# Kernel optimization log

Hardware: AMD Instinct MI355X
Metric: run time of the kernel (lower is better)

## Reference

```python
import jax, jax.numpy as jnp
import numpy as np
from jax import lax

N, L, E, ED, H = 100000, 48, 1600000, 17, 48

def _lin_init(k, fan_in, fan_out):
    kw, kb = jax.random.split(k)
    s = 1.0 / np.sqrt(fan_in)
    W = jax.random.uniform(kw, (fan_in, fan_out), minval=-s, maxval=s, dtype=jnp.float32)
    b = jax.random.uniform(kb, (fan_out,), minval=-s, maxval=s, dtype=jnp.float32)
    return W, b

def setup_inputs() -> dict:
    key = jax.random.key(0)
    ks = jax.random.split(key, 10)
    nodes = jax.random.normal(ks[0], (N, L, 1), dtype=jnp.float32)
    edge_index = jax.random.randint(ks[1], (2, E), 0, N, dtype=jnp.int64) if jax.config.jax_enable_x64 else jax.random.randint(ks[1], (2, E), 0, N, dtype=jnp.int32)
    edge_attr = jax.random.normal(ks[2], (E, ED), dtype=jnp.float32)
    valid = (jax.random.uniform(ks[3], (1, N, L)) < 0.8).astype(jnp.float32)
    r = jnp.zeros((1,), jnp.float32)
    fx = jnp.zeros((1,), jnp.float32)
    W1, b1 = _lin_init(ks[4], ED, H)   # lin_edge[0]
    W2, b2 = _lin_init(ks[5], H, H)    # lin_edge[2]
    Wg, bg = _lin_init(ks[6], H, H)    # gru[0]
    Ww, bw = _lin_init(ks[7], H, 1)    # weight_mlp
    Wf, bf = _lin_init(ks[8], 3, 1)    # fuse_mlp
    return {"nodes": nodes, "edge_index": edge_index, "edge_attr": edge_attr,
            "valid": valid, "r": r, "fx": fx,
            "W1": W1, "b1": b1, "W2": W2, "b2": b2, "Wg": Wg, "bg": bg,
            "Ww": Ww, "bw": bw, "Wf": Wf, "bf": bf}

def _gelu(x):
    return jax.nn.gelu(x, approximate=False)  # torch GELU default is exact erf

def reference(nodes, edge_index, edge_attr, valid, r, fx,
              W1, b1, W2, b2, Wg, bg, Ww, bw, Wf, bf):
    n = nodes.shape[0]
    # torch.no_grad block: mask nodes by valid, flatten (C==1)
    v = lax.stop_gradient(valid[0][..., None])            # [N, L, 1]
    x = lax.stop_gradient((nodes * v).reshape(n, L))      # [N, L]
    original = x
    nv_mask = (1.0 - v).reshape(n, L)                     # not_valid mask [N, L]
    src, dst = edge_index[0], edge_index[1]
    for _ in range(3):
        # lin_edge: 17 -> 48 -> GELU -> 48 -> ReLU  (per edge)
        eh = jax.nn.relu(_gelu(edge_attr @ W1 + b1) @ W2 + b2)      # [E, 48]
        xc = jnp.concatenate([x, v[..., 0]], axis=-1)               # [N, 2L]
        x_j = xc[src]                                               # gather [E, 2L]
        g = _gelu(eh @ Wg + bg)                                     # gru
        w = g @ Ww + bw                                             # [E, 1]
        w = jnp.mean(x_j[:, L:], axis=-1, keepdims=True) * w
        msg = x_j * jax.nn.sigmoid(w)                               # [E, 2L]
        agg = jax.ops.segment_sum(msg, dst, num_segments=n)         # scatter-add [N, 2L]
        new_half = agg[:, :L]                                       # [N, L]
        nn3 = jnp.stack([new_half, x, nv_mask], axis=-1)            # [N, L, 3]
        mask = jax.nn.sigmoid((nn3 @ Wf + bf)[..., 0])              # [N, L]
        x = (1.0 - mask) * x + nv_mask * mask * new_half
        v = jnp.logical_or((original != x)[..., None], v > 0).astype(jnp.float32)
        v = v.at[:, 0].set(0.0)
        nv_mask = (1.0 - v).reshape(n, L)
    return x[0][None]  # [1, L]
```

## Files before the change

kernel.cpp:

```cpp
#include <hip/hip_runtime.h>
#include <math.h>

#define NN 100000
#define LF 48
#define NE 1600000
#define EDIMS 17
#define MASKW 3125
#define CAP_E 16384
#define MAXLOC 12288

static_assert(NN == MASKW * 32, "mask width");
static_assert((CAP_E & (CAP_E - 1)) == 0, "CAP_E pow2");

__device__ __forceinline__ float gelu_f(float x) {
    return 0.5f * x * (1.0f + erff(x * 0.7071067811865475f));
}
__device__ __forceinline__ float sigm_f(float x) {
    return 1.0f / (1.0f + expf(-x));
}

__global__ void seed_kernel(unsigned* __restrict__ M3) {
    if (threadIdx.x == 0 && blockIdx.x == 0) M3[0] = 1u;
}

__global__ void expand_kernel(const int* __restrict__ src, const int* __restrict__ dst,
                              const unsigned* __restrict__ Min, unsigned* __restrict__ Mout,
                              int4* __restrict__ list, int* __restrict__ counter)
{
    int e = blockIdx.x * 256 + threadIdx.x;
    if (e >= NE) return;
    int d = dst[e];
    if (Min[d >> 5] & (1u << (d & 31))) {
        int s = src[e];
        int idx = atomicAdd(counter, 1);
        if (idx < CAP_E) list[idx] = make_int4(s, d, e, 0);
        atomicOr(&Mout[s >> 5], 1u << (s & 31));
    }
}

__global__ void compact_kernel(const unsigned* __restrict__ M0, int* __restrict__ n2l,
                               int* __restrict__ l2n, int* __restrict__ nloc)
{
    int w = blockIdx.x * 256 + threadIdx.x;
    if (w >= MASKW) return;
    unsigned bits = M0[w];
    while (bits) {
        int b = __ffs(bits) - 1;
        bits &= bits - 1;
        int node = w * 32 + b;
        int loc = atomicAdd(nloc, 1);
        if (loc < MAXLOC) { n2l[node] = loc; l2n[loc] = node; }
    }
}

__global__ void init_kernel(const int* __restrict__ nloc_p, const int* __restrict__ l2n,
                            const float* __restrict__ nodes, const float* __restrict__ valid,
                            float* __restrict__ X0, float* __restrict__ V0, float* __restrict__ MV0)
{
    int loc = blockIdx.x * 256 + threadIdx.x;
    int nl = *nloc_p; if (nl > MAXLOC) nl = MAXLOC;
    if (loc >= nl) return;
    int node = l2n[loc];
    float sum = 0.f;
    #pragma unroll 4
    for (int l = 0; l < LF; ++l) {
        float v = valid[node * LF + l];
        float x = nodes[node * LF + l] * v;
        X0[loc * LF + l] = x;
        V0[loc * LF + l] = v;
        sum += v;
    }
    MV0[loc] = sum * (1.0f / 48.0f);
}

__global__ void w0_kernel(int4* __restrict__ lists, const int* __restrict__ counts,
                          const int* __restrict__ n2l, const float* __restrict__ ea_g,
                          const float* __restrict__ W1, const float* __restrict__ b1,
                          const float* __restrict__ W2, const float* __restrict__ b2,
                          const float* __restrict__ Wg, const float* __restrict__ bg,
                          const float* __restrict__ Ww, const float* __restrict__ bw)
{
    int t = blockIdx.x >> 14;
    int i = blockIdx.x & (CAP_E - 1);
    int c = counts[t]; if (c > CAP_E) c = CAP_E;
    if (i >= c) return;
    int4 ent = lists[t * CAP_E + i];
    __shared__ float sh[64];
    __shared__ float eas[EDIMS];
    int lane = threadIdx.x;
    if (lane < EDIMS) eas[lane] = ea_g[(long)ent.z * EDIMS + lane];
    __syncthreads();
    float h1 = 0.f;
    if (lane < 48) {
        float acc = b1[lane];
        #pragma unroll
        for (int k = 0; k < EDIMS; ++k) acc += eas[k] * W1[k * 48 + lane];
        h1 = gelu_f(acc);
    }
    sh[lane] = h1;
    __syncthreads();
    float h2 = 0.f;
    if (lane < 48) {
        float acc = b2[lane];
        #pragma unroll 8
        for (int k = 0; k < 48; ++k) acc += sh[k] * W2[k * 48 + lane];
        h2 = fmaxf(acc, 0.f);
    }
    __syncthreads();
    sh[lane] = h2;
    __syncthreads();
    float part = 0.f;
    if (lane < 48) {
        float acc = bg[lane];
        #pragma unroll 8
        for (int k = 0; k < 48; ++k) acc += sh[k] * Wg[k * 48 + lane];
        part = gelu_f(acc) * Ww[lane];
    }
    #pragma unroll
    for (int offd = 32; offd > 0; offd >>= 1) part += __shfl_down(part, offd, 64);
    if (lane == 0) {
        float w0 = part + bw[0];
        int sl = n2l[ent.x]; if ((unsigned)sl >= MAXLOC) sl = 0;
        int dl = n2l[ent.y]; if ((unsigned)dl >= MAXLOC) dl = 0;
        lists[t * CAP_E + i] = make_int4(sl, dl, ent.z, __float_as_int(w0));
    }
}

__global__ void edge_agg_kernel(const int4* __restrict__ list, const int* __restrict__ count_p,
                                const float* __restrict__ Xprev, const float* __restrict__ MVprev,
                                float* __restrict__ agg)
{
    int gid = blockIdx.x * 256 + threadIdx.x;
    int i = gid >> 6, lane = gid & 63;
    int c = *count_p; if (c > CAP_E) c = CAP_E;
    if (i >= c || lane >= 48) return;
    int4 ent = list[i];
    if ((unsigned)ent.x >= MAXLOC || (unsigned)ent.y >= MAXLOC) return;
    float s = sigm_f(MVprev[ent.x] * __int_as_float(ent.w));
    atomicAdd(&agg[ent.y * 48 + lane], s * Xprev[ent.x * 48 + lane]);
}

__global__ void node_update_kernel(const int* __restrict__ nloc_p, const int* __restrict__ l2n,
                                   const unsigned* __restrict__ Mt,
                                   const float* __restrict__ agg, const float* __restrict__ Xprev,
                                   const float* __restrict__ Vprev, const float* __restrict__ Xorig,
                                   float* __restrict__ Xcur, float* __restrict__ Vcur,
                                   float* __restrict__ MVcur,
                                   const float* __restrict__ Wf, const float* __restrict__ bf)
{
    int loc = blockIdx.x * 256 + threadIdx.x;
    int nl = *nloc_p; if (nl > MAXLOC) nl = MAXLOC;
    if (loc >= nl) return;
    int node = l2n[loc];
    if (!(Mt[node >> 5] & (1u << (node & 31)))) return;
    float wf0 = Wf[0], wf1 = Wf[1], wf2 = Wf[2], bfs = bf[0];
    float vsum = 0.f;
    #pragma unroll 4
    for (int l = 0; l < LF; ++l) {
        float nh = agg[loc * LF + l];
        float xo = Xprev[loc * LF + l];
        float vp = Vprev[loc * LF + l];
        float nv = 1.0f - vp;
        float m = sigm_f(nh * wf0 + xo * wf1 + nv * wf2 + bfs);
        float xn = (1.0f - m) * xo + nv * m * nh;
        float vn = ((Xorig[loc * LF + l] != xn) || (vp > 0.f)) ? 1.0f : 0.0f;
        if (l == 0) vn = 0.0f;
        Xcur[loc * LF + l] = xn;
        Vcur[loc * LF + l] = vn;
        vsum += vn;
    }
    MVcur[loc] = vsum * (1.0f / 48.0f);
}

__global__ void output_kernel(const int* __restrict__ n2l, const float* __restrict__ Xf,
                              float* __restrict__ out)
{
    int l = threadIdx.x;
    if (l < 48) out[l] = Xf[n2l[0] * 48 + l];
}

extern "C" void kernel_launch(void* const* d_in, const int* in_sizes, int n_in,
                              void* d_out, int out_size, void* d_ws, size_t ws_size,
                              hipStream_t stream)
{
    const float* nodes = (const float*)d_in[0];
    const int*   eidx  = (const int*)d_in[1];
    const float* eattr = (const float*)d_in[2];
    const float* valid = (const float*)d_in[3];
    const float* W1 = (const float*)d_in[6];
    const float* b1 = (const float*)d_in[7];
    const float* W2 = (const float*)d_in[8];
    const float* b2 = (const float*)d_in[9];
    const float* Wg = (const float*)d_in[10];
    const float* bg = (const float*)d_in[11];
    const float* Ww = (const float*)d_in[12];
    const float* bw = (const float*)d_in[13];
    const float* Wf = (const float*)d_in[14];
    const float* bf = (const float*)d_in[15];
    const int* src = eidx;
    const int* dst = eidx + NE;

    char* ws = (char*)d_ws;
    size_t off = 0;
    auto alloc = [&](size_t bytes) -> char* {
        char* p = ws + off;
        off += (bytes + 255) & ~(size_t)255;
        return p;
    };
    int*      counters = (int*)alloc(64);
    unsigned* M3 = (unsigned*)alloc(MASKW * 4);
    unsigned* M2 = (unsigned*)alloc(MASKW * 4);
    unsigned* M1 = (unsigned*)alloc(MASKW * 4);
    unsigned* M0 = (unsigned*)alloc(MASKW * 4);
    int*      n2l = (int*)alloc((size_t)NN * 4);
    int*      l2n = (int*)alloc((size_t)MAXLOC * 4);
    int4*     lists = (int4*)alloc((size_t)3 * CAP_E * 16);
    float*    X0 = (float*)alloc((size_t)MAXLOC * LF * 4);
    float*    XA = (float*)alloc((size_t)MAXLOC * LF * 4);
    float*    XB = (float*)alloc((size_t)MAXLOC * LF * 4);
    float*    VA = (float*)alloc((size_t)MAXLOC * LF * 4);
    float*    VB = (float*)alloc((size_t)MAXLOC * LF * 4);
    float*    MVA = (float*)alloc((size_t)MAXLOC * 4);
    float*    MVB = (float*)alloc((size_t)MAXLOC * 4);
    float*    agg = (float*)alloc((size_t)MAXLOC * LF * 4);
    if (off > ws_size) return;

    hipMemsetAsync(counters, 0, 64, stream);
    hipMemsetAsync(M3, 0, MASKW * 4, stream);
    hipMemsetAsync(M2, 0, MASKW * 4, stream);
    hipMemsetAsync(M1, 0, MASKW * 4, stream);
    hipMemsetAsync(M0, 0, MASKW * 4, stream);
    seed_kernel<<<1, 64, 0, stream>>>(M3);

    hipMemcpyAsync(M2, M3, MASKW * 4, hipMemcpyDeviceToDevice, stream);
    expand_kernel<<<NE / 256, 256, 0, stream>>>(src, dst, M3, M2, lists + 0 * CAP_E, counters + 0);
    hipMemcpyAsync(M1, M2, MASKW * 4, hipMemcpyDeviceToDevice, stream);
    expand_kernel<<<NE / 256, 256, 0, stream>>>(src, dst, M2, M1, lists + 1 * CAP_E, counters + 1);
    hipMemcpyAsync(M0, M1, MASKW * 4, hipMemcpyDeviceToDevice, stream);
    expand_kernel<<<NE / 256, 256, 0, stream>>>(src, dst, M1, M0, lists + 2 * CAP_E, counters + 2);

    compact_kernel<<<(MASKW + 255) / 256, 256, 0, stream>>>(M0, n2l, l2n, counters + 3);
    init_kernel<<<MAXLOC / 256, 256, 0, stream>>>(counters + 3, l2n, nodes, valid, X0, VA, MVA);
    w0_kernel<<<3 * CAP_E, 64, 0, stream>>>(lists, counters, n2l, eattr,
                                            W1, b1, W2, b2, Wg, bg, Ww, bw);

    const size_t aggBytes = (size_t)MAXLOC * LF * 4;
    hipMemsetAsync(agg, 0, aggBytes, stream);
    edge_agg_kernel<<<CAP_E * 64 / 256, 256, 0, stream>>>(lists + 2 * CAP_E, counters + 2, X0, MVA, agg);
    node_update_kernel<<<MAXLOC / 256, 256, 0, stream>>>(counters + 3, l2n, M1, agg, X0, VA, X0,
                                                         XA, VB, MVB, Wf, bf);
    hipMemsetAsync(agg, 0, aggBytes, stream);
    edge_agg_kernel<<<CAP_E * 64 / 256, 256, 0, stream>>>(lists + 1 * CAP_E, counters + 1, XA, MVB, agg);
    node_update_kernel<<<MAXLOC / 256, 256, 0, stream>>>(counters + 3, l2n, M2, agg, XA, VB, X0,
                                                         XB, VA, MVA, Wf, bf);
    hipMemsetAsync(agg, 0, aggBytes, stream);
    edge_agg_kernel<<<CAP_E * 64 / 256, 256, 0, stream>>>(lists + 0 * CAP_E, counters + 0, XB, MVA, agg);
    node_update_kernel<<<MAXLOC / 256, 256, 0, stream>>>(counters + 3, l2n, M3, agg, XB, VA, X0,
                                                         XA, VB, MVB, Wf, bf);

    output_kernel<<<1, 64, 0, stream>>>(n2l, XA, (float*)d_out);
}
```

Baseline: 351.0 us.

## Fuse all phases into one cooperative persistent kernel with grid syncs

```diff
diff --git a/kernel.cpp b/kernel.cpp
--- a/kernel.cpp
+++ b/kernel.cpp
@@ -1,5 +1,8 @@
 #include <hip/hip_runtime.h>
+#include <hip/hip_cooperative_groups.h>
 #include <math.h>
+
+namespace cg = cooperative_groups;
 
 #define NN 100000
 #define LF 48
@@ -8,10 +11,25 @@
 #define MASKW 3125
 #define CAP_E 16384
 #define MAXLOC 12288
+#define BLK 256
+#define GRID_MAX 1024
 
 static_assert(NN == MASKW * 32, "mask width");
 static_assert((CAP_E & (CAP_E - 1)) == 0, "CAP_E pow2");
 
+struct Params {
+    const float* nodes; const float* valid; const float* eattr;
+    const int* src; const int* dst;
+    const float *W1, *b1, *W2, *b2, *Wg, *bg, *Ww, *bw, *Wf, *bf;
+    int* counters;
+    unsigned *M3, *M2, *M1, *M0;
+    int *n2l, *l2n;
+    int4* lists;
+    float *X0, *XA, *XB, *VA, *VB, *MVA, *MVB;
+    float *agg;
+    float* out;
+};
+
 __device__ __forceinline__ float gelu_f(float x) {
     return 0.5f * x * (1.0f + erff(x * 0.7071067811865475f));
 }
@@ -19,244 +37,252 @@
     return 1.0f / (1.0f + expf(-x));
 }
 
-__global__ void seed_kernel(unsigned* __restrict__ M3) {
-    if (threadIdx.x == 0 && blockIdx.x == 0) M3[0] = 1u;
-}
-
-__global__ void expand_kernel(const int* __restrict__ src, const int* __restrict__ dst,
-                              const unsigned* __restrict__ Min, unsigned* __restrict__ Mout,
-                              int4* __restrict__ list, int* __restrict__ counter)
-{
-    int e = blockIdx.x * 256 + threadIdx.x;
-    if (e >= NE) return;
-    int d = dst[e];
-    if (Min[d >> 5] & (1u << (d & 31))) {
-        int s = src[e];
-        int idx = atomicAdd(counter, 1);
-        if (idx < CAP_E) list[idx] = make_int4(s, d, e, 0);
-        atomicOr(&Mout[s >> 5], 1u << (s & 31));
-    }
-}
-
-__global__ void compact_kernel(const unsigned* __restrict__ M0, int* __restrict__ n2l,
-                               int* __restrict__ l2n, int* __restrict__ nloc)
-{
-    int w = blockIdx.x * 256 + threadIdx.x;
-    if (w >= MASKW) return;
-    unsigned bits = M0[w];
-    while (bits) {
-        int b = __ffs(bits) - 1;
-        bits &= bits - 1;
-        int node = w * 32 + b;
-        int loc = atomicAdd(nloc, 1);
-        if (loc < MAXLOC) { n2l[node] = loc; l2n[loc] = node; }
-    }
-}
-
-__global__ void init_kernel(const int* __restrict__ nloc_p, const int* __restrict__ l2n,
-                            const float* __restrict__ nodes, const float* __restrict__ valid,
-                            float* __restrict__ X0, float* __restrict__ V0, float* __restrict__ MV0)
-{
-    int loc = blockIdx.x * 256 + threadIdx.x;
-    int nl = *nloc_p; if (nl > MAXLOC) nl = MAXLOC;
-    if (loc >= nl) return;
-    int node = l2n[loc];
-    float sum = 0.f;
-    #pragma unroll 4
-    for (int l = 0; l < LF; ++l) {
-        float v = valid[node * LF + l];
-        float x = nodes[node * LF + l] * v;
-        X0[loc * LF + l] = x;
-        V0[loc * LF + l] = v;
-        sum += v;
-    }
-    MV0[loc] = sum * (1.0f / 48.0f);
-}
-
-__global__ void w0_kernel(int4* __restrict__ lists, const int* __restrict__ counts,
-                          const int* __restrict__ n2l, const float* __restrict__ ea_g,
-                          const float* __restrict__ W1, const float* __restrict__ b1,
-                          const float* __restrict__ W2, const float* __restrict__ b2,
-                          const float* __restrict__ Wg, const float* __restrict__ bg,
-                          const float* __restrict__ Ww, const float* __restrict__ bw)
-{
-    int t = blockIdx.x >> 14;
-    int i = blockIdx.x & (CAP_E - 1);
-    int c = counts[t]; if (c > CAP_E) c = CAP_E;
-    if (i >= c) return;
-    int4 ent = lists[t * CAP_E + i];
-    __shared__ float sh[64];
-    __shared__ float eas[EDIMS];
-    int lane = threadIdx.x;
-    if (lane < EDIMS) eas[lane] = ea_g[(long)ent.z * EDIMS + lane];
-    __syncthreads();
+
+__device__ void expand_phase(const Params& p, const unsigned* __restrict__ Min,
+                             unsigned* __restrict__ Mout, int4* __restrict__ list,
+                             int* __restrict__ counter, int tid, int nthr)
+{
+    for (int w = tid; w < MASKW; w += nthr) atomicOr(&Mout[w], Min[w]);
+    for (int e = tid; e < NE; e += nthr) {
+        int d = p.dst[e];
+        if (Min[d >> 5] & (1u << (d & 31))) {
+            int s = p.src[e];
+            int idx = atomicAdd(counter, 1);
+            if (idx < CAP_E) list[idx] = make_int4(s, d, e, 0);
+            atomicOr(&Mout[s >> 5], 1u << (s & 31));
+        }
+    }
+}
+
+__device__ void w0_edge(const Params& p, int4* __restrict__ entp, int lane)
+{
+    int4 ent = *entp;
+    float ea = 0.f;
+    if (lane < EDIMS) ea = p.eattr[(long)ent.z * EDIMS + lane];
     float h1 = 0.f;
     if (lane < 48) {
-        float acc = b1[lane];
+        float acc = p.b1[lane];
         #pragma unroll
-        for (int k = 0; k < EDIMS; ++k) acc += eas[k] * W1[k * 48 + lane];
+        for (int k = 0; k < EDIMS; ++k) acc += __shfl(ea, k, 64) * p.W1[k * 48 + lane];
         h1 = gelu_f(acc);
     }
-    sh[lane] = h1;
-    __syncthreads();
     float h2 = 0.f;
     if (lane < 48) {
-        float acc = b2[lane];
+        float acc = p.b2[lane];
         #pragma unroll 8
-        for (int k = 0; k < 48; ++k) acc += sh[k] * W2[k * 48 + lane];
+        for (int k = 0; k < 48; ++k) acc += __shfl(h1, k, 64) * p.W2[k * 48 + lane];
         h2 = fmaxf(acc, 0.f);
     }
-    __syncthreads();
-    sh[lane] = h2;
-    __syncthreads();
     float part = 0.f;
     if (lane < 48) {
-        float acc = bg[lane];
+        float acc = p.bg[lane];
         #pragma unroll 8
-        for (int k = 0; k < 48; ++k) acc += sh[k] * Wg[k * 48 + lane];
-        part = gelu_f(acc) * Ww[lane];
+        for (int k = 0; k < 48; ++k) acc += __shfl(h2, k, 64) * p.Wg[k * 48 + lane];
+        part = gelu_f(acc) * p.Ww[lane];
     }
     #pragma unroll
-    for (int offd = 32; offd > 0; offd >>= 1) part += __shfl_down(part, offd, 64);
+    for (int off = 32; off > 0; off >>= 1) part += __shfl_down(part, off, 64);
     if (lane == 0) {
-        float w0 = part + bw[0];
-        int sl = n2l[ent.x]; if ((unsigned)sl >= MAXLOC) sl = 0;
-        int dl = n2l[ent.y]; if ((unsigned)dl >= MAXLOC) dl = 0;
-        lists[t * CAP_E + i] = make_int4(sl, dl, ent.z, __float_as_int(w0));
-    }
-}
-
-__global__ void edge_agg_kernel(const int4* __restrict__ list, const int* __restrict__ count_p,
-                                const float* __restrict__ Xprev, const float* __restrict__ MVprev,
-                                float* __restrict__ agg)
-{
-    int gid = blockIdx.x * 256 + threadIdx.x;
-    int i = gid >> 6, lane = gid & 63;
-    int c = *count_p; if (c > CAP_E) c = CAP_E;
-    if (i >= c || lane >= 48) return;
-    int4 ent = list[i];
-    if ((unsigned)ent.x >= MAXLOC || (unsigned)ent.y >= MAXLOC) return;
-    float s = sigm_f(MVprev[ent.x] * __int_as_float(ent.w));
-    atomicAdd(&agg[ent.y * 48 + lane], s * Xprev[ent.x * 48 + lane]);
-}
-
-__global__ void node_update_kernel(const int* __restrict__ nloc_p, const int* __restrict__ l2n,
-                                   const unsigned* __restrict__ Mt,
-                                   const float* __restrict__ agg, const float* __restrict__ Xprev,
-                                   const float* __restrict__ Vprev, const float* __restrict__ Xorig,
-                                   float* __restrict__ Xcur, float* __restrict__ Vcur,
-                                   float* __restrict__ MVcur,
-                                   const float* __restrict__ Wf, const float* __restrict__ bf)
-{
-    int loc = blockIdx.x * 256 + threadIdx.x;
-    int nl = *nloc_p; if (nl > MAXLOC) nl = MAXLOC;
-    if (loc >= nl) return;
-    int node = l2n[loc];
-    if (!(Mt[node >> 5] & (1u << (node & 31)))) return;
-    float wf0 = Wf[0], wf1 = Wf[1], wf2 = Wf[2], bfs = bf[0];
-    float vsum = 0.f;
-    #pragma unroll 4
-    for (int l = 0; l < LF; ++l) {
-        float nh = agg[loc * LF + l];
-        float xo = Xprev[loc * LF + l];
-        float vp = Vprev[loc * LF + l];
-        float nv = 1.0f - vp;
-        float m = sigm_f(nh * wf0 + xo * wf1 + nv * wf2 + bfs);
-        float xn = (1.0f - m) * xo + nv * m * nh;
-        float vn = ((Xorig[loc * LF + l] != xn) || (vp > 0.f)) ? 1.0f : 0.0f;
-        if (l == 0) vn = 0.0f;
-        Xcur[loc * LF + l] = xn;
-        Vcur[loc * LF + l] = vn;
-        vsum += vn;
-    }
-    MVcur[loc] = vsum * (1.0f / 48.0f);
-}
-
-__global__ void output_kernel(const int* __restrict__ n2l, const float* __restrict__ Xf,
-                              float* __restrict__ out)
-{
-    int l = threadIdx.x;
-    if (l < 48) out[l] = Xf[n2l[0] * 48 + l];
+        float w0 = part + p.bw[0];
+        int sl = p.n2l[ent.x]; if ((unsigned)sl >= MAXLOC) sl = 0;
+        int dl = p.n2l[ent.y]; if ((unsigned)dl >= MAXLOC) dl = 0;
+        *entp = make_int4(sl, dl, ent.z, __float_as_int(w0));
+    }
+}
+
+__device__ void agg_phase(const Params& p, const int4* __restrict__ list,
+                          const int* __restrict__ cnt, const float* __restrict__ Xprev,
+                          const float* __restrict__ MVprev, float* __restrict__ agg,
+                          int tid, int nthr)
+{
+    int c = *cnt; if (c > CAP_E) c = CAP_E;
+    int lane = tid & 63;
+    for (int i = tid >> 6; i < c; i += (nthr >> 6)) {
+        int4 ent = list[i];
+        if ((unsigned)ent.x >= MAXLOC || (unsigned)ent.y >= MAXLOC) continue;
+        float s = sigm_f(MVprev[ent.x] * __int_as_float(ent.w));
+        if (lane < 48) atomicAdd(&agg[ent.y * LF + lane], s * Xprev[ent.x * LF + lane]);
+    }
+}
+
+__device__ void update_phase(const Params& p, const unsigned* __restrict__ Mt,
+                             const float* __restrict__ agg, const float* __restrict__ Xprev,
+                             const float* __restrict__ Vprev, float* __restrict__ Xcur,
+                             float* __restrict__ Vcur, float* __restrict__ MVcur,
+                             int tid, int nthr)
+{
+    int nl = p.counters[3]; if (nl > MAXLOC) nl = MAXLOC;
+    float wf0 = p.Wf[0], wf1 = p.Wf[1], wf2 = p.Wf[2], bfs = p.bf[0];
+    for (int loc = tid; loc < nl; loc += nthr) {
+        int node = p.l2n[loc];
+        if (!(Mt[node >> 5] & (1u << (node & 31)))) continue;
+        float vsum = 0.f;
+        #pragma unroll 4
+        for (int l = 0; l < LF; ++l) {
+            float nh = agg[loc * LF + l];
+            float xo = Xprev[loc * LF + l];
+            float vp = Vprev[loc * LF + l];
+            float nv = 1.0f - vp;
+            float m = sigm_f(nh * wf0 + xo * wf1 + nv * wf2 + bfs);
+            float xn = (1.0f - m) * xo + nv * m * nh;
+            float vn = ((p.X0[loc * LF + l] != xn) || (vp > 0.f)) ? 1.0f : 0.0f;
+            if (l == 0) vn = 0.0f;
+            Xcur[loc * LF + l] = xn;
+            Vcur[loc * LF + l] = vn;
+            vsum += vn;
+        }
+        MVcur[loc] = vsum * (1.0f / 48.0f);
+    }
+}
+
+__device__ void run_phase(const Params& p, int ph, int tid, int nthr)
+{
+    float* agg0 = p.agg;
+    float* agg1 = p.agg + MAXLOC * LF;
+    float* agg2 = p.agg + 2 * MAXLOC * LF;
+    switch (ph) {
+    case 0: {
+        if (tid < 4) p.counters[tid] = 0;
+        for (int i = tid; i < MASKW; i += nthr) {
+            p.M3[i] = (i == 0) ? 1u : 0u;
+            p.M2[i] = 0u; p.M1[i] = 0u; p.M0[i] = 0u;
+        }
+        for (int i = tid; i < 3 * MAXLOC * LF; i += nthr) p.agg[i] = 0.f;
+    } break;
+    case 1: expand_phase(p, p.M3, p.M2, p.lists + 0 * CAP_E, p.counters + 0, tid, nthr); break;
+    case 2: expand_phase(p, p.M2, p.M1, p.lists + 1 * CAP_E, p.counters + 1, tid, nthr); break;
+    case 3: expand_phase(p, p.M1, p.M0, p.lists + 2 * CAP_E, p.counters + 2, tid, nthr); break;
+    case 4: {
+        for (int w = tid; w < MASKW; w += nthr) {
+            unsigned bits = p.M0[w];
+            while (bits) {
+                int b = __ffs(bits) - 1;
+                bits &= bits - 1;
+                int node = w * 32 + b;
+                int loc = atomicAdd(p.counters + 3, 1);
+                if (loc < MAXLOC) { p.n2l[node] = loc; p.l2n[loc] = node; }
+            }
+        }
+    } break;
+    case 5: {
+        int nl = p.counters[3]; if (nl > MAXLOC) nl = MAXLOC;
+        for (int loc = tid; loc < nl; loc += nthr) {
+            int node = p.l2n[loc];
+            const float4* nv = (const float4*)(p.valid + (size_t)node * LF);
+            const float4* nx = (const float4*)(p.nodes + (size_t)node * LF);
+            float4* X0v = (float4*)(p.X0 + (size_t)loc * LF);
+            float4* V0v = (float4*)(p.VA + (size_t)loc * LF);
+            float sum = 0.f;
+            #pragma unroll
+            for (int k = 0; k < 12; ++k) {
+                float4 v = nv[k], x = nx[k];
+                x.x *= v.x; x.y *= v.y; x.z *= v.z; x.w *= v.w;
+                X0v[k] = x; V0v[k] = v;
+                sum += v.x + v.y + v.z + v.w;
+            }
+            p.MVA[loc] = sum * (1.0f / 48.0f);
+        }
+        int c0 = p.counters[0]; c0 = (c0 > CAP_E) ? CAP_E : c0;
+        int c1 = p.counters[1]; c1 = (c1 > CAP_E) ? CAP_E : c1;
+        int c2 = p.counters[2]; c2 = (c2 > CAP_E) ? CAP_E : c2;
+        int total = c0 + c1 + c2;
+        int lane = tid & 63;
+        for (int g = tid >> 6; g < total; g += (nthr >> 6)) {
+            int4* entp;
+            if (g < c0)           entp = p.lists + g;
+            else if (g < c0 + c1) entp = p.lists + CAP_E + (g - c0);
+            else                  entp = p.lists + 2 * CAP_E + (g - c0 - c1);
+            w0_edge(p, entp, lane);
+        }
+    } break;
+    case 6:  agg_phase(p, p.lists + 2 * CAP_E, p.counters + 2, p.X0, p.MVA, agg0, tid, nthr); break;
+    case 7:  update_phase(p, p.M1, agg0, p.X0, p.VA, p.XA, p.VB, p.MVB, tid, nthr); break;
+    case 8:  agg_phase(p, p.lists + 1 * CAP_E, p.counters + 1, p.XA, p.MVB, agg1, tid, nthr); break;
+    case 9:  update_phase(p, p.M2, agg1, p.XA, p.VB, p.XB, p.VA, p.MVA, tid, nthr); break;
+    case 10: agg_phase(p, p.lists + 0 * CAP_E, p.counters + 0, p.XB, p.MVA, agg2, tid, nthr); break;
+    case 11: update_phase(p, p.M3, agg2, p.XB, p.VA, p.XA, p.VB, p.MVB, tid, nthr); break;
+    case 12: {
+        if (tid < 48) p.out[tid] = p.XA[(size_t)p.n2l[0] * 48 + tid];
+    } break;
+    }
+}
+
+__global__ void __launch_bounds__(BLK, 4) fused_kernel(Params p)
+{
+    cg::grid_group grid = cg::this_grid();
+    int tid = blockIdx.x * BLK + threadIdx.x;
+    int nthr = (int)gridDim.x * BLK;
+    for (int ph = 0; ph < 13; ++ph) {
+        run_phase(p, ph, tid, nthr);
+        if (ph < 12) grid.sync();
+    }
+}
+
+__global__ void __launch_bounds__(BLK) phase_kernel(Params p, int ph)
+{
+    run_phase(p, ph, blockIdx.x * BLK + threadIdx.x, (int)gridDim.x * BLK);
 }
 
 extern "C" void kernel_launch(void* const* d_in, const int* in_sizes, int n_in,
                               void* d_out, int out_size, void* d_ws, size_t ws_size,
                               hipStream_t stream)
 {
+    (void)in_sizes; (void)n_in; (void)out_size;
     const float* nodes = (const float*)d_in[0];
     const int*   eidx  = (const int*)d_in[1];
     const float* eattr = (const float*)d_in[2];
     const float* valid = (const float*)d_in[3];
-    const float* W1 = (const float*)d_in[6];
-    const float* b1 = (const float*)d_in[7];
-    const float* W2 = (const float*)d_in[8];
-    const float* b2 = (const float*)d_in[9];
-    const float* Wg = (const float*)d_in[10];
-    const float* bg = (const float*)d_in[11];
-    const float* Ww = (const float*)d_in[12];
-    const float* bw = (const float*)d_in[13];
-    const float* Wf = (const float*)d_in[14];
-    const float* bf = (const float*)d_in[15];
-    const int* src = eidx;
-    const int* dst = eidx + NE;
+    Params hp;
+    hp.nodes = nodes; hp.valid = valid; hp.eattr = eattr;
+    hp.src = eidx; hp.dst = eidx + NE;
+    hp.W1 = (const float*)d_in[6];  hp.b1 = (const float*)d_in[7];
+    hp.W2 = (const float*)d_in[8];  hp.b2 = (const float*)d_in[9];
+    hp.Wg = (const float*)d_in[10]; hp.bg = (const float*)d_in[11];
+    hp.Ww = (const float*)d_in[12]; hp.bw = (const float*)d_in[13];
+    hp.Wf = (const float*)d_in[14]; hp.bf = (const float*)d_in[15];
 
     char* ws = (char*)d_ws;
     size_t off = 0;
     auto alloc = [&](size_t bytes) -> char* {
-        char* p = ws + off;
+        char* ptr = ws + off;
         off += (bytes + 255) & ~(size_t)255;
-        return p;
+        return ptr;
     };
-    int*      counters = (int*)alloc(64);
-    unsigned* M3 = (unsigned*)alloc(MASKW * 4);
-    unsigned* M2 = (unsigned*)alloc(MASKW * 4);
-    unsigned* M1 = (unsigned*)alloc(MASKW * 4);
-    unsigned* M0 = (unsigned*)alloc(MASKW * 4);
-    int*      n2l = (int*)alloc((size_t)NN * 4);
-    int*      l2n = (int*)alloc((size_t)MAXLOC * 4);
-    int4*     lists = (int4*)alloc((size_t)3 * CAP_E * 16);
-    float*    X0 = (float*)alloc((size_t)MAXLOC * LF * 4);
-    float*    XA = (float*)alloc((size_t)MAXLOC * LF * 4);
-    float*    XB = (float*)alloc((size_t)MAXLOC * LF * 4);
-    float*    VA = (float*)alloc((size_t)MAXLOC * LF * 4);
-    float*    VB = (float*)alloc((size_t)MAXLOC * LF * 4);
-    float*    MVA = (float*)alloc((size_t)MAXLOC * 4);
-    float*    MVB = (float*)alloc((size_t)MAXLOC * 4);
-    float*    agg = (float*)alloc((size_t)MAXLOC * LF * 4);
+    hp.counters = (int*)alloc(64);
+    hp.M3 = (unsigned*)alloc(MASKW * 4);
+    hp.M2 = (unsigned*)alloc(MASKW * 4);
+    hp.M1 = (unsigned*)alloc(MASKW * 4);
+    hp.M0 = (unsigned*)alloc(MASKW * 4);
+    hp.n2l = (int*)alloc((size_t)NN * 4);
+    hp.l2n = (int*)alloc((size_t)MAXLOC * 4);
+    hp.lists = (int4*)alloc((size_t)3 * CAP_E * 16);
+    hp.X0 = (float*)alloc((size_t)MAXLOC * LF * 4);
+    hp.XA = (float*)alloc((size_t)MAXLOC * LF * 4);
+    hp.XB = (float*)alloc((size_t)MAXLOC * LF * 4);
+    hp.VA = (float*)alloc((size_t)MAXLOC * LF * 4);
+    hp.VB = (float*)alloc((size_t)MAXLOC * LF * 4);
+    hp.MVA = (float*)alloc((size_t)MAXLOC * 4);
+    hp.MVB = (float*)alloc((size_t)MAXLOC * 4);
+    hp.agg = (float*)alloc((size_t)3 * MAXLOC * LF * 4);
+    hp.out = (float*)d_out;
     if (off > ws_size) return;
 
-    hipMemsetAsync(counters, 0, 64, stream);
-    hipMemsetAsync(M3, 0, MASKW * 4, stream);
-    hipMemsetAsync(M2, 0, MASKW * 4, stream);
-    hipMemsetAsync(M1, 0, MASKW * 4, stream);
-    hipMemsetAsync(M0, 0, MASKW * 4, stream);
-    seed_kernel<<<1, 64, 0, stream>>>(M3);
-
-    hipMemcpyAsync(M2, M3, MASKW * 4, hipMemcpyDeviceToDevice, stream);
-    expand_kernel<<<NE / 256, 256, 0, stream>>>(src, dst, M3, M2, lists + 0 * CAP_E, counters + 0);
-    hipMemcpyAsync(M1, M2, MASKW * 4, hipMemcpyDeviceToDevice, stream);
-    expand_kernel<<<NE / 256, 256, 0, stream>>>(src, dst, M2, M1, lists + 1 * CAP_E, counters + 1);
-    hipMemcpyAsync(M0, M1, MASKW * 4, hipMemcpyDeviceToDevice, stream);
-    expand_kernel<<<NE / 256, 256, 0, stream>>>(src, dst, M1, M0, lists + 2 * CAP_E, counters + 2);
-
-    compact_kernel<<<(MASKW + 255) / 256, 256, 0, stream>>>(M0, n2l, l2n, counters + 3);
-    init_kernel<<<MAXLOC / 256, 256, 0, stream>>>(counters + 3, l2n, nodes, valid, X0, VA, MVA);
-    w0_kernel<<<3 * CAP_E, 64, 0, stream>>>(lists, counters, n2l, eattr,
-                                            W1, b1, W2, b2, Wg, bg, Ww, bw);
-
-    const size_t aggBytes = (size_t)MAXLOC * LF * 4;
-    hipMemsetAsync(agg, 0, aggBytes, stream);
-    edge_agg_kernel<<<CAP_E * 64 / 256, 256, 0, stream>>>(lists + 2 * CAP_E, counters + 2, X0, MVA, agg);
-    node_update_kernel<<<MAXLOC / 256, 256, 0, stream>>>(counters + 3, l2n, M1, agg, X0, VA, X0,
-                                                         XA, VB, MVB, Wf, bf);
-    hipMemsetAsync(agg, 0, aggBytes, stream);
-    edge_agg_kernel<<<CAP_E * 64 / 256, 256, 0, stream>>>(lists + 1 * CAP_E, counters + 1, XA, MVB, agg);
-    node_update_kernel<<<MAXLOC / 256, 256, 0, stream>>>(counters + 3, l2n, M2, agg, XA, VB, X0,
-                                                         XB, VA, MVA, Wf, bf);
-    hipMemsetAsync(agg, 0, aggBytes, stream);
-    edge_agg_kernel<<<CAP_E * 64 / 256, 256, 0, stream>>>(lists + 0 * CAP_E, counters + 0, XB, MVA, agg);
-    node_update_kernel<<<MAXLOC / 256, 256, 0, stream>>>(counters + 3, l2n, M3, agg, XB, VA, X0,
-                                                         XA, VB, MVB, Wf, bf);
-
-    output_kernel<<<1, 64, 0, stream>>>(n2l, XA, (float*)d_out);
-}
+    int grid = GRID_MAX;
+    int maxBlk = 0;
+    if (hipOccupancyMaxActiveBlocksPerMultiprocessor(
+            &maxBlk, reinterpret_cast<const void*>(&fused_kernel), BLK, 0) == hipSuccess
+        && maxBlk > 0) {
+        int cap = maxBlk * 256;
+        if (grid > cap) grid = cap;
+        if (grid < 1) grid = 1;
+    }
+
+    void* args[] = { &hp };
+    hipError_t err = hipLaunchCooperativeKernel(
+        reinterpret_cast<const void*>(&fused_kernel),
+        dim3(grid), dim3(BLK), args, 0, stream);
+    if (err != hipSuccess) {
+        for (int ph = 0; ph < 13; ++ph)
+            phase_kernel<<<GRID_MAX, BLK, 0, stream>>>(hp, ph);
+    }
+}
```

Result: slower. 1.011 ms (+188.1%).

## Fuse launches: merge init/w0, collapse tail rounds into one block, drop memsets

Applied to the files above, without the earlier changes.

```diff
diff --git a/kernel.cpp b/kernel.cpp
--- a/kernel.cpp
+++ b/kernel.cpp
@@ -8,9 +8,9 @@
 #define MASKW 3125
 #define CAP_E 16384
 #define MAXLOC 12288
+#define EB 1563
 
 static_assert(NN == MASKW * 32, "mask width");
-static_assert((CAP_E & (CAP_E - 1)) == 0, "CAP_E pow2");
 
 __device__ __forceinline__ float gelu_f(float x) {
     return 0.5f * x * (1.0f + erff(x * 0.7071067811865475f));
@@ -19,22 +19,78 @@
     return 1.0f / (1.0f + expf(-x));
 }
 
-__global__ void seed_kernel(unsigned* __restrict__ M3) {
-    if (threadIdx.x == 0 && blockIdx.x == 0) M3[0] = 1u;
+__global__ void expand1_kernel(const int* __restrict__ src, const int* __restrict__ dst,
+                               unsigned* __restrict__ M2, unsigned* __restrict__ M1,
+                               unsigned* __restrict__ M0, float4* __restrict__ aggz,
+                               int4* __restrict__ list0, int* __restrict__ counter)
+{
+    int tid = blockIdx.x * 256 + threadIdx.x;
+    int nthr = (int)gridDim.x * 256;
+    for (int i = tid; i < MASKW; i += nthr) { M1[i] = 0u; M0[i] = 0u; }
+    for (int i = tid; i < (3 * MAXLOC * LF) / 4; i += nthr)
+        aggz[i] = make_float4(0.f, 0.f, 0.f, 0.f);
+    if (tid == 0) atomicOr(&M2[0], 1u);
+    int e0 = tid * 4;
+    if (e0 + 3 < NE) {
+        int4 d4 = *(const int4*)(dst + e0);
+        int dv[4] = { d4.x, d4.y, d4.z, d4.w };
+        #pragma unroll
+        for (int k = 0; k < 4; ++k) {
+            if (dv[k] == 0) {
+                int e = e0 + k;
+                int s = src[e];
+                int idx = atomicAdd(counter, 1);
+                if (idx < CAP_E) list0[idx] = make_int4(s, 0, e, 0);
+                atomicOr(&M2[s >> 5], 1u << (s & 31));
+            }
+        }
+    } else {
+        for (int e = e0; e < NE; ++e) {
+            if (dst[e] == 0) {
+                int s = src[e];
+                int idx = atomicAdd(counter, 1);
+                if (idx < CAP_E) list0[idx] = make_int4(s, 0, e, 0);
+                atomicOr(&M2[s >> 5], 1u << (s & 31));
+            }
+        }
+    }
 }
 
 __global__ void expand_kernel(const int* __restrict__ src, const int* __restrict__ dst,
                               const unsigned* __restrict__ Min, unsigned* __restrict__ Mout,
                               int4* __restrict__ list, int* __restrict__ counter)
 {
-    int e = blockIdx.x * 256 + threadIdx.x;
-    if (e >= NE) return;
-    int d = dst[e];
-    if (Min[d >> 5] & (1u << (d & 31))) {
-        int s = src[e];
-        int idx = atomicAdd(counter, 1);
-        if (idx < CAP_E) list[idx] = make_int4(s, d, e, 0);
-        atomicOr(&Mout[s >> 5], 1u << (s & 31));
+    int tid = blockIdx.x * 256 + threadIdx.x;
+    int nthr = (int)gridDim.x * 256;
+    for (int i = tid; i < MASKW; i += nthr) {
+        unsigned m = Min[i];
+        if (m) atomicOr(&Mout[i], m);
+    }
+    int e0 = tid * 4;
+    if (e0 + 3 < NE) {
+        int4 d4 = *(const int4*)(dst + e0);
+        int dv[4] = { d4.x, d4.y, d4.z, d4.w };
+        #pragma unroll
+        for (int k = 0; k < 4; ++k) {
+            int d = dv[k];
+            if (Min[d >> 5] & (1u << (d & 31))) {
+                int e = e0 + k;
+                int s = src[e];
+                int idx = atomicAdd(counter, 1);
+                if (idx < CAP_E) list[idx] = make_int4(s, d, e, 0);
+                atomicOr(&Mout[s >> 5], 1u << (s & 31));
+            }
+        }
+    } else {
+        for (int e = e0; e < NE; ++e) {
+            int d = dst[e];
+            if (Min[d >> 5] & (1u << (d & 31))) {
+                int s = src[e];
+                int idx = atomicAdd(counter, 1);
+                if (idx < CAP_E) list[idx] = make_int4(s, d, e, 0);
+                atomicOr(&Mout[s >> 5], 1u << (s & 31));
+            }
+        }
     }
 }
 
@@ -53,136 +109,189 @@
     }
 }
 
-__global__ void init_kernel(const int* __restrict__ nloc_p, const int* __restrict__ l2n,
-                            const float* __restrict__ nodes, const float* __restrict__ valid,
-                            float* __restrict__ X0, float* __restrict__ V0, float* __restrict__ MV0)
-{
-    int loc = blockIdx.x * 256 + threadIdx.x;
-    int nl = *nloc_p; if (nl > MAXLOC) nl = MAXLOC;
-    if (loc >= nl) return;
-    int node = l2n[loc];
-    float sum = 0.f;
-    #pragma unroll 4
-    for (int l = 0; l < LF; ++l) {
-        float v = valid[node * LF + l];
-        float x = nodes[node * LF + l] * v;
-        X0[loc * LF + l] = x;
-        V0[loc * LF + l] = v;
-        sum += v;
-    }
-    MV0[loc] = sum * (1.0f / 48.0f);
-}
-
-__global__ void w0_kernel(int4* __restrict__ lists, const int* __restrict__ counts,
-                          const int* __restrict__ n2l, const float* __restrict__ ea_g,
-                          const float* __restrict__ W1, const float* __restrict__ b1,
-                          const float* __restrict__ W2, const float* __restrict__ b2,
-                          const float* __restrict__ Wg, const float* __restrict__ bg,
-                          const float* __restrict__ Ww, const float* __restrict__ bw)
-{
-    int t = blockIdx.x >> 14;
-    int i = blockIdx.x & (CAP_E - 1);
-    int c = counts[t]; if (c > CAP_E) c = CAP_E;
-    if (i >= c) return;
-    int4 ent = lists[t * CAP_E + i];
-    __shared__ float sh[64];
-    __shared__ float eas[EDIMS];
-    int lane = threadIdx.x;
-    if (lane < EDIMS) eas[lane] = ea_g[(long)ent.z * EDIMS + lane];
-    __syncthreads();
+__device__ void w0_edge(int4* __restrict__ entp, const int* __restrict__ n2l,
+                        const float* __restrict__ ea_g,
+                        const float* __restrict__ W1, const float* __restrict__ b1,
+                        const float* __restrict__ W2, const float* __restrict__ b2,
+                        const float* __restrict__ Wg, const float* __restrict__ bg,
+                        const float* __restrict__ Ww, const float* __restrict__ bw,
+                        int lane)
+{
+    int4 ent = *entp;
+    float ea = 0.f;
+    if (lane < EDIMS) ea = ea_g[(long)ent.z * EDIMS + lane];
     float h1 = 0.f;
     if (lane < 48) {
         float acc = b1[lane];
         #pragma unroll
-        for (int k = 0; k < EDIMS; ++k) acc += eas[k] * W1[k * 48 + lane];
+        for (int k = 0; k < EDIMS; ++k) acc += __shfl(ea, k, 64) * W1[k * 48 + lane];
         h1 = gelu_f(acc);
     }
-    sh[lane] = h1;
-    __syncthreads();
     float h2 = 0.f;
     if (lane < 48) {
         float acc = b2[lane];
         #pragma unroll 8
-        for (int k = 0; k < 48; ++k) acc += sh[k] * W2[k * 48 + lane];
+        for (int k = 0; k < 48; ++k) acc += __shfl(h1, k, 64) * W2[k * 48 + lane];
         h2 = fmaxf(acc, 0.f);
     }
-    __syncthreads();
-    sh[lane] = h2;
-    __syncthreads();
     float part = 0.f;
     if (lane < 48) {
         float acc = bg[lane];
         #pragma unroll 8
-        for (int k = 0; k < 48; ++k) acc += sh[k] * Wg[k * 48 + lane];
+        for (int k = 0; k < 48; ++k) acc += __shfl(h2, k, 64) * Wg[k * 48 + lane];
         part = gelu_f(acc) * Ww[lane];
     }
     #pragma unroll
-    for (int offd = 32; offd > 0; offd >>= 1) part += __shfl_down(part, offd, 64);
+    for (int off = 32; off > 0; off >>= 1) part += __shfl_down(part, off, 64);
     if (lane == 0) {
         float w0 = part + bw[0];
         int sl = n2l[ent.x]; if ((unsigned)sl >= MAXLOC) sl = 0;
         int dl = n2l[ent.y]; if ((unsigned)dl >= MAXLOC) dl = 0;
-        lists[t * CAP_E + i] = make_int4(sl, dl, ent.z, __float_as_int(w0));
-    }
-}
-
-__global__ void edge_agg_kernel(const int4* __restrict__ list, const int* __restrict__ count_p,
-                                const float* __restrict__ Xprev, const float* __restrict__ MVprev,
-                                float* __restrict__ agg)
-{
-    int gid = blockIdx.x * 256 + threadIdx.x;
-    int i = gid >> 6, lane = gid & 63;
-    int c = *count_p; if (c > CAP_E) c = CAP_E;
-    if (i >= c || lane >= 48) return;
-    int4 ent = list[i];
-    if ((unsigned)ent.x >= MAXLOC || (unsigned)ent.y >= MAXLOC) return;
-    float s = sigm_f(MVprev[ent.x] * __int_as_float(ent.w));
-    atomicAdd(&agg[ent.y * 48 + lane], s * Xprev[ent.x * 48 + lane]);
-}
-
-__global__ void node_update_kernel(const int* __restrict__ nloc_p, const int* __restrict__ l2n,
-                                   const unsigned* __restrict__ Mt,
-                                   const float* __restrict__ agg, const float* __restrict__ Xprev,
-                                   const float* __restrict__ Vprev, const float* __restrict__ Xorig,
-                                   float* __restrict__ Xcur, float* __restrict__ Vcur,
-                                   float* __restrict__ MVcur,
-                                   const float* __restrict__ Wf, const float* __restrict__ bf)
-{
-    int loc = blockIdx.x * 256 + threadIdx.x;
-    int nl = *nloc_p; if (nl > MAXLOC) nl = MAXLOC;
-    if (loc >= nl) return;
-    int node = l2n[loc];
-    if (!(Mt[node >> 5] & (1u << (node & 31)))) return;
+        *entp = make_int4(sl, dl, ent.z, __float_as_int(w0));
+    }
+}
+
+__global__ void initw0_kernel(const int* __restrict__ counters, const int* __restrict__ l2n,
+                              const int* __restrict__ n2l,
+                              const float* __restrict__ nodes, const float* __restrict__ valid,
+                              float* __restrict__ X0, float* __restrict__ V0,
+                              float* __restrict__ MV0,
+                              int4* __restrict__ lists, const float* __restrict__ ea_g,
+                              const float* __restrict__ W1, const float* __restrict__ b1,
+                              const float* __restrict__ W2, const float* __restrict__ b2,
+                              const float* __restrict__ Wg, const float* __restrict__ bg,
+                              const float* __restrict__ Ww, const float* __restrict__ bw)
+{
+    int tid = blockIdx.x * 256 + threadIdx.x;
+    int nthr = (int)gridDim.x * 256;
+    int nl = counters[3]; if (nl > MAXLOC) nl = MAXLOC;
+    for (int loc = tid; loc < nl; loc += nthr) {
+        int node = l2n[loc];
+        const float4* nv = (const float4*)(valid + (size_t)node * LF);
+        const float4* nx = (const float4*)(nodes + (size_t)node * LF);
+        float4* X0v = (float4*)(X0 + (size_t)loc * LF);
+        float4* V0v = (float4*)(V0 + (size_t)loc * LF);
+        float sum = 0.f;
+        #pragma unroll
+        for (int k = 0; k < 12; ++k) {
+            float4 v = nv[k], x = nx[k];
+            x.x *= v.x; x.y *= v.y; x.z *= v.z; x.w *= v.w;
+            X0v[k] = x; V0v[k] = v;
+            sum += v.x + v.y + v.z + v.w;
+        }
+        MV0[loc] = sum * (1.0f / 48.0f);
+    }
+    int c0 = counters[0]; c0 = (c0 > CAP_E) ? CAP_E : c0;
+    int c1 = counters[1]; c1 = (c1 > CAP_E) ? CAP_E : c1;
+    int c2 = counters[2]; c2 = (c2 > CAP_E) ? CAP_E : c2;
+    int total = c0 + c1 + c2;
+    int lane = tid & 63;
+    for (int g = tid >> 6; g < total; g += (nthr >> 6)) {
+        int4* entp;
+        if (g < c0)           entp = lists + g;
+        else if (g < c0 + c1) entp = lists + CAP_E + (g - c0);
+        else                  entp = lists + 2 * CAP_E + (g - c0 - c1);
+        w0_edge(entp, n2l, ea_g, W1, b1, W2, b2, Wg, bg, Ww, bw, lane);
+    }
+}
+
+__global__ void agg1_kernel(const int4* __restrict__ list, const int* __restrict__ cnt,
+                            const float* __restrict__ Xprev, const float* __restrict__ MVprev,
+                            float* __restrict__ agg)
+{
+    int tid = blockIdx.x * 256 + threadIdx.x;
+    int nthr = (int)gridDim.x * 256;
+    int c = *cnt; if (c > CAP_E) c = CAP_E;
+    int lane = tid & 63;
+    for (int i = tid >> 6; i < c; i += (nthr >> 6)) {
+        int4 ent = list[i];
+        if ((unsigned)ent.x >= MAXLOC || (unsigned)ent.y >= MAXLOC) continue;
+        float s = sigm_f(MVprev[ent.x] * __int_as_float(ent.w));
+        if (lane < 48) atomicAdd(&agg[ent.y * LF + lane], s * Xprev[ent.x * LF + lane]);
+    }
+}
+
+
+__device__ void upd_block(int nl, const int* __restrict__ l2n, const unsigned* __restrict__ Mt,
+                          float* __restrict__ agg, const float* __restrict__ Xp,
+                          const float* __restrict__ Vp, const float* __restrict__ Xorig,
+                          float* __restrict__ Xc, float* __restrict__ Vc, float* __restrict__ MVc,
+                          float wf0, float wf1, float wf2, float bfs, int tid)
+{
+    for (int loc = tid; loc < nl; loc += 1024) {
+        int node = l2n[loc];
+        if (!(Mt[node >> 5] & (1u << (node & 31)))) continue;
+        float vsum = 0.f;
+        #pragma unroll 4
+        for (int l = 0; l < LF; ++l) {
+            float nh = atomicAdd(&agg[loc * LF + l], 0.f);
+            float xo = Xp[loc * LF + l];
+            float vp = Vp[loc * LF + l];
+            float nv = 1.0f - vp;
+            float m = sigm_f(nh * wf0 + xo * wf1 + nv * wf2 + bfs);
+            float xn = (1.0f - m) * xo + nv * m * nh;
+            float vn = ((Xorig[loc * LF + l] != xn) || (vp > 0.f)) ? 1.0f : 0.0f;
+            if (l == 0) vn = 0.0f;
+            Xc[loc * LF + l] = xn;
+            Vc[loc * LF + l] = vn;
+            vsum += vn;
+        }
+        MVc[loc] = vsum * (1.0f / 48.0f);
+    }
+}
+
+__device__ void agg_block(const int4* __restrict__ list, int c, const float* __restrict__ Xp,
+                          const float* __restrict__ MVp, float* __restrict__ agg, int tid)
+{
+    int lane = tid & 63;
+    for (int i = tid >> 6; i < c; i += 16) {
+        int4 ent = list[i];
+        if ((unsigned)ent.x >= MAXLOC || (unsigned)ent.y >= MAXLOC) continue;
+        float s = sigm_f(MVp[ent.x] * __int_as_float(ent.w));
+        if (lane < 48) atomicAdd(&agg[ent.y * LF + lane], s * Xp[ent.x * LF + lane]);
+    }
+}
+
+__global__ void __launch_bounds__(1024) tail_kernel(
+    const int* __restrict__ counters, const int* __restrict__ l2n, const int* __restrict__ n2l,
+    const unsigned* __restrict__ M1, const unsigned* __restrict__ M2,
+    const int4* __restrict__ lists, const float* __restrict__ X0,
+    float* __restrict__ XA, float* __restrict__ XB,
+    float* __restrict__ VA, float* __restrict__ VB,
+    float* __restrict__ MVA, float* __restrict__ MVB,
+    float* __restrict__ agg0, float* __restrict__ agg1b, float* __restrict__ agg2b,
+    const float* __restrict__ Wf, const float* __restrict__ bf, float* __restrict__ out)
+{
+    int tid = threadIdx.x;
+    int nl = counters[3]; if (nl > MAXLOC) nl = MAXLOC;
+    int c0 = counters[0]; c0 = (c0 > CAP_E) ? CAP_E : c0;
+    int c1 = counters[1]; c1 = (c1 > CAP_E) ? CAP_E : c1;
     float wf0 = Wf[0], wf1 = Wf[1], wf2 = Wf[2], bfs = bf[0];
-    float vsum = 0.f;
-    #pragma unroll 4
-    for (int l = 0; l < LF; ++l) {
-        float nh = agg[loc * LF + l];
-        float xo = Xprev[loc * LF + l];
-        float vp = Vprev[loc * LF + l];
+
+    upd_block(nl, l2n, M1, agg0, X0, VA, X0, XA, VB, MVB, wf0, wf1, wf2, bfs, tid);
+    __syncthreads();
+    agg_block(lists + CAP_E, c1, XA, MVB, agg1b, tid);
+    __syncthreads();
+    upd_block(nl, l2n, M2, agg1b, XA, VB, X0, XB, VA, MVA, wf0, wf1, wf2, bfs, tid);
+    __syncthreads();
+    agg_block(lists, c0, XB, MVA, agg2b, tid);
+    __syncthreads();
+    if (tid < 48) {
+        int loc0 = n2l[0]; if ((unsigned)loc0 >= MAXLOC) loc0 = 0;
+        float nh = atomicAdd(&agg2b[loc0 * LF + tid], 0.f);
+        float xo = XB[loc0 * LF + tid];
+        float vp = VA[loc0 * LF + tid];
         float nv = 1.0f - vp;
         float m = sigm_f(nh * wf0 + xo * wf1 + nv * wf2 + bfs);
-        float xn = (1.0f - m) * xo + nv * m * nh;
-        float vn = ((Xorig[loc * LF + l] != xn) || (vp > 0.f)) ? 1.0f : 0.0f;
-        if (l == 0) vn = 0.0f;
-        Xcur[loc * LF + l] = xn;
-        Vcur[loc * LF + l] = vn;
-        vsum += vn;
-    }
-    MVcur[loc] = vsum * (1.0f / 48.0f);
-}
-
-__global__ void output_kernel(const int* __restrict__ n2l, const float* __restrict__ Xf,
-                              float* __restrict__ out)
-{
-    int l = threadIdx.x;
-    if (l < 48) out[l] = Xf[n2l[0] * 48 + l];
+        out[tid] = (1.0f - m) * xo + nv * m * nh;
+    }
 }
 
 extern "C" void kernel_launch(void* const* d_in, const int* in_sizes, int n_in,
                               void* d_out, int out_size, void* d_ws, size_t ws_size,
                               hipStream_t stream)
 {
+    (void)in_sizes; (void)n_in; (void)out_size;
     const float* nodes = (const float*)d_in[0];
     const int*   eidx  = (const int*)d_in[1];
     const float* eattr = (const float*)d_in[2];
@@ -207,9 +316,9 @@
         off += (bytes + 255) & ~(size_t)255;
         return p;
     };
-    int*      counters = (int*)alloc(64);
-    unsigned* M3 = (unsigned*)alloc(MASKW * 4);
-    unsigned* M2 = (unsigned*)alloc(MASKW * 4);
+    char*     zb = alloc(256 + MASKW * 4);
+    int*      counters = (int*)zb;
+    unsigned* M2 = (unsigned*)(zb + 256);
     unsigned* M1 = (unsigned*)alloc(MASKW * 4);
     unsigned* M0 = (unsigned*)alloc(MASKW * 4);
     int*      n2l = (int*)alloc((size_t)NN * 4);
@@ -222,41 +331,24 @@
     float*    VB = (float*)alloc((size_t)MAXLOC * LF * 4);
     float*    MVA = (float*)alloc((size_t)MAXLOC * 4);
     float*    MVB = (float*)alloc((size_t)MAXLOC * 4);
-    float*    agg = (float*)alloc((size_t)MAXLOC * LF * 4);
+    float*    agg = (float*)alloc((size_t)3 * MAXLOC * LF * 4);
     if (off > ws_size) return;
-
-    hipMemsetAsync(counters, 0, 64, stream);
-    hipMemsetAsync(M3, 0, MASKW * 4, stream);
-    hipMemsetAsync(M2, 0, MASKW * 4, stream);
-    hipMemsetAsync(M1, 0, MASKW * 4, stream);
-    hipMemsetAsync(M0, 0, MASKW * 4, stream);
-    seed_kernel<<<1, 64, 0, stream>>>(M3);
-
-    hipMemcpyAsync(M2, M3, MASKW * 4, hipMemcpyDeviceToDevice, stream);
-    expand_kernel<<<NE / 256, 256, 0, stream>>>(src, dst, M3, M2, lists + 0 * CAP_E, counters + 0);
-    hipMemcpyAsync(M1, M2, MASKW * 4, hipMemcpyDeviceToDevice, stream);
-    expand_kernel<<<NE / 256, 256, 0, stream>>>(src, dst, M2, M1, lists + 1 * CAP_E, counters + 1);
-    hipMemcpyAsync(M0, M1, MASKW * 4, hipMemcpyDeviceToDevice, stream);
-    expand_kernel<<<NE / 256, 256, 0, stream>>>(src, dst, M1, M0, lists + 2 * CAP_E, counters + 2);
-
+    float* agg0  = agg;
+    float* agg1b = agg + MAXLOC * LF;
+    float* agg2b = agg + 2 * MAXLOC * LF;
+
+    hipMemsetAsync(zb, 0, 256 + MASKW * 4, stream);
+
+    expand1_kernel<<<EB, 256, 0, stream>>>(src, dst, M2, M1, M0, (float4*)agg,
+                                           lists + 0 * CAP_E, counters + 0);
+    expand_kernel<<<EB, 256, 0, stream>>>(src, dst, M2, M1, lists + 1 * CAP_E, counters + 1);
+    expand_kernel<<<EB, 256, 0, stream>>>(src, dst, M1, M0, lists + 2 * CAP_E, counters + 2);
     compact_kernel<<<(MASKW + 255) / 256, 256, 0, stream>>>(M0, n2l, l2n, counters + 3);
-    init_kernel<<<MAXLOC / 256, 256, 0, stream>>>(counters + 3, l2n, nodes, valid, X0, VA, MVA);
-    w0_kernel<<<3 * CAP_E, 64, 0, stream>>>(lists, counters, n2l, eattr,
+    initw0_kernel<<<1024, 256, 0, stream>>>(counters, l2n, n2l, nodes, valid,
+                                            X0, VA, MVA, lists, eattr,
                                             W1, b1, W2, b2, Wg, bg, Ww, bw);
-
-    const size_t aggBytes = (size_t)MAXLOC * LF * 4;
-    hipMemsetAsync(agg, 0, aggBytes, stream);
-    edge_agg_kernel<<<CAP_E * 64 / 256, 256, 0, stream>>>(lists + 2 * CAP_E, counters + 2, X0, MVA, agg);
-    node_update_kernel<<<MAXLOC / 256, 256, 0, stream>>>(counters + 3, l2n, M1, agg, X0, VA, X0,
-                                                         XA, VB, MVB, Wf, bf);
-    hipMemsetAsync(agg, 0, aggBytes, stream);
-    edge_agg_kernel<<<CAP_E * 64 / 256, 256, 0, stream>>>(lists + 1 * CAP_E, counters + 1, XA, MVB, agg);
-    node_update_kernel<<<MAXLOC / 256, 256, 0, stream>>>(counters + 3, l2n, M2, agg, XA, VB, X0,
-                                                         XB, VA, MVA, Wf, bf);
-    hipMemsetAsync(agg, 0, aggBytes, stream);
-    edge_agg_kernel<<<CAP_E * 64 / 256, 256, 0, stream>>>(lists + 0 * CAP_E, counters + 0, XB, MVA, agg);
-    node_update_kernel<<<MAXLOC / 256, 256, 0, stream>>>(counters + 3, l2n, M3, agg, XB, VA, X0,
-                                                         XA, VB, MVB, Wf, bf);
-
-    output_kernel<<<1, 64, 0, stream>>>(n2l, XA, (float*)d_out);
-}
+    agg1_kernel<<<1024, 256, 0, stream>>>(lists + 2 * CAP_E, counters + 2, X0, MVA, agg0);
+    tail_kernel<<<1, 1024, 0, stream>>>(counters, l2n, n2l, M1, M2, lists, X0,
+                                        XA, XB, VA, VB, MVA, MVB,
+                                        agg0, agg1b, agg2b, Wf, bf, (float*)d_out);
+}
```

Result: slower. 395.9 us (+12.8%).
